# Kernel optimization log

Measured on AMD Instinct MI355X. Metric: run time of the kernel, lower is better.

The kernel has to match this reference:

```python
import jax, jax.numpy as jnp
import numpy as np

L = 4
VOCAB = 258  # 256 codes + 2 (pad/cls)
D = 512
B, T = 64, 1024


def setup_inputs() -> dict:
    key = jax.random.key(0)
    k1, k2, k3, k4 = jax.random.split(key, 4)
    level_ids = jax.random.randint(k1, (B, T), 0, L, dtype=jnp.int64)
    token_ids = jax.random.randint(k2, (B, T), 0, VOCAB, dtype=jnp.int64)
    # per-level embedding tables stacked: [L, VOCAB, D] (all vocab sizes equal)
    emb_tables = jax.random.normal(k3, (L, VOCAB, D), dtype=jnp.float32)
    level_embed = jax.random.normal(k4, (L, D), dtype=jnp.float32)
    return {"level_ids": level_ids, "token_ids": token_ids,
            "emb_tables": emb_tables, "level_embed": level_embed}


def reference(level_ids, token_ids, emb_tables, level_embed):
    # Fused form of the per-level masked gather/scatter: each (b,t) position
    # reads row token_ids[b,t] from table level_ids[b,t], then adds the
    # level embedding for that level. Dropout p=0.0 -> identity.
    out = emb_tables[level_ids, token_ids] + level_embed[level_ids]  # [B,T,D]
    return out
```

## Files before the change

kernel.cpp:

```cpp
#include <hip/hip_runtime.h>


#define MLE_D     512
#define MLE_D4    128
#define MLE_VOCAB 258

__global__ __launch_bounds__(256) void MultiLevelEmbedding_34437047780006_kernel(
    const int* __restrict__ level_ids,
    const int* __restrict__ token_ids,
    const float* __restrict__ emb_tables,
    const float* __restrict__ level_embed,
    float* __restrict__ out,
    long long total_f4)
{
    long long stride = (long long)gridDim.x * blockDim.x;
    for (long long i = (long long)blockIdx.x * blockDim.x + threadIdx.x;
         i < total_f4; i += stride) {
        int row = (int)(i >> 7);
        int d4  = (int)(i & 127);
        int lvl = level_ids[row];
        int tok = token_ids[row];
        const float4* tab = reinterpret_cast<const float4*>(
            emb_tables + ((long long)lvl * MLE_VOCAB + (long long)tok) * MLE_D);
        const float4* lev = reinterpret_cast<const float4*>(
            level_embed + (long long)lvl * MLE_D);
        float4 a = tab[d4];
        float4 b = lev[d4];
        float4 o;
        o.x = a.x + b.x;
        o.y = a.y + b.y;
        o.z = a.z + b.z;
        o.w = a.w + b.w;
        reinterpret_cast<float4*>(out)[i] = o;
    }
}

extern "C" void kernel_launch(void* const* d_in, const int* in_sizes, int n_in,
                              void* d_out, int out_size, void* d_ws, size_t ws_size,
                              hipStream_t stream) {
    const int*   level_ids   = (const int*)d_in[0];
    const int*   token_ids   = (const int*)d_in[1];
    const float* emb_tables  = (const float*)d_in[2];
    const float* level_embed = (const float*)d_in[3];
    float*       out         = (float*)d_out;

    int n_rows = in_sizes[0];
    long long total_f4 = (long long)n_rows * MLE_D4;

    const int block = 256;
    long long want_blocks = (total_f4 + block - 1) / block;
    int grid = (int)(want_blocks < 2048 ? want_blocks : 2048);

    MultiLevelEmbedding_34437047780006_kernel<<<grid, block, 0, stream>>>(
        level_ids, token_ids, emb_tables, level_embed, out, total_f4);
}
```

Baseline: 31.91 us.

## Map one wavefront per row with scalar index loads and nontemporal stores

Restructures the gather so each 64-lane wavefront handles a whole 512-float row, with the level and token ids read once and broadcast through readfirstlane instead of being reloaded per float4. The loop is unrolled to process two rows per iteration so more loads are in flight, and output writes use nontemporal stores to avoid polluting the cache. Total traffic is about 128MB of writes plus table reads that mostly hit in cache, so the kernel is write-bound and the expected gain is limited.

```diff
diff --git a/kernel.cpp b/kernel.cpp
--- a/kernel.cpp
+++ b/kernel.cpp
@@ -5,33 +5,67 @@
 #define MLE_D4    128
 #define MLE_VOCAB 258
 
+typedef float f32x4 __attribute__((ext_vector_type(4)));
+
 __global__ __launch_bounds__(256) void MultiLevelEmbedding_34437047780006_kernel(
     const int* __restrict__ level_ids,
     const int* __restrict__ token_ids,
     const float* __restrict__ emb_tables,
     const float* __restrict__ level_embed,
     float* __restrict__ out,
-    long long total_f4)
+    int nrows)
 {
-    long long stride = (long long)gridDim.x * blockDim.x;
-    for (long long i = (long long)blockIdx.x * blockDim.x + threadIdx.x;
-         i < total_f4; i += stride) {
-        int row = (int)(i >> 7);
-        int d4  = (int)(i & 127);
-        int lvl = level_ids[row];
-        int tok = token_ids[row];
-        const float4* tab = reinterpret_cast<const float4*>(
-            emb_tables + ((long long)lvl * MLE_VOCAB + (long long)tok) * MLE_D);
-        const float4* lev = reinterpret_cast<const float4*>(
-            level_embed + (long long)lvl * MLE_D);
-        float4 a = tab[d4];
-        float4 b = lev[d4];
-        float4 o;
-        o.x = a.x + b.x;
-        o.y = a.y + b.y;
-        o.z = a.z + b.z;
-        o.w = a.w + b.w;
-        reinterpret_cast<float4*>(out)[i] = o;
+    const int lane = (int)(threadIdx.x & 63);
+    const int wib  = __builtin_amdgcn_readfirstlane((int)(threadIdx.x >> 6));
+    const int nw   = (int)gridDim.x * 4;
+    int gw = (int)blockIdx.x * 4 + wib;
+
+    const f32x4* __restrict__ levv = reinterpret_cast<const f32x4*>(level_embed);
+
+    int row = gw;
+    for (; row + nw < nrows; row += 2 * nw) {
+        const int r0 = row;
+        const int r1 = row + nw;
+        const int lvl0 = __builtin_amdgcn_readfirstlane(level_ids[r0]);
+        const int tok0 = __builtin_amdgcn_readfirstlane(token_ids[r0]);
+        const int lvl1 = __builtin_amdgcn_readfirstlane(level_ids[r1]);
+        const int tok1 = __builtin_amdgcn_readfirstlane(token_ids[r1]);
+
+        const f32x4* __restrict__ t0 = reinterpret_cast<const f32x4*>(
+            emb_tables + (long long)(lvl0 * MLE_VOCAB + tok0) * MLE_D);
+        const f32x4* __restrict__ t1 = reinterpret_cast<const f32x4*>(
+            emb_tables + (long long)(lvl1 * MLE_VOCAB + tok1) * MLE_D);
+
+        f32x4 a0 = t0[lane];
+        f32x4 b0 = t0[lane + 64];
+        f32x4 a1 = t1[lane];
+        f32x4 b1 = t1[lane + 64];
+
+        f32x4 la0 = levv[lvl0 * MLE_D4 + lane];
+        f32x4 lb0 = levv[lvl0 * MLE_D4 + lane + 64];
+        f32x4 la1 = levv[lvl1 * MLE_D4 + lane];
+        f32x4 lb1 = levv[lvl1 * MLE_D4 + lane + 64];
+
+        f32x4* __restrict__ o0 = reinterpret_cast<f32x4*>(out + (long long)r0 * MLE_D);
+        f32x4* __restrict__ o1 = reinterpret_cast<f32x4*>(out + (long long)r1 * MLE_D);
+
+        __builtin_nontemporal_store(a0 + la0, o0 + lane);
+        __builtin_nontemporal_store(b0 + lb0, o0 + lane + 64);
+        __builtin_nontemporal_store(a1 + la1, o1 + lane);
+        __builtin_nontemporal_store(b1 + lb1, o1 + lane + 64);
+    }
+    for (; row < nrows; row += nw) {
+        const int lvl = __builtin_amdgcn_readfirstlane(level_ids[row]);
+        const int tok = __builtin_amdgcn_readfirstlane(token_ids[row]);
+        const f32x4* __restrict__ t = reinterpret_cast<const f32x4*>(
+            emb_tables + (long long)(lvl * MLE_VOCAB + tok) * MLE_D);
+        f32x4 a = t[lane];
+        f32x4 b = t[lane + 64];
+        f32x4 la = levv[lvl * MLE_D4 + lane];
+        f32x4 lb = levv[lvl * MLE_D4 + lane + 64];
+        f32x4* __restrict__ o = reinterpret_cast<f32x4*>(out + (long long)row * MLE_D);
+        __builtin_nontemporal_store(a + la, o + lane);
+        __builtin_nontemporal_store(b + lb, o + lane + 64);
     }
 }
 
@@ -44,13 +78,13 @@
     const float* level_embed = (const float*)d_in[3];
     float*       out         = (float*)d_out;
 
-    int n_rows = in_sizes[0];
-    long long total_f4 = (long long)n_rows * MLE_D4;
+    const int nrows = in_sizes[0];
 
     const int block = 256;
-    long long want_blocks = (total_f4 + block - 1) / block;
-    int grid = (int)(want_blocks < 2048 ? want_blocks : 2048);
+    int grid = 2048;
+    int max_blocks = (nrows + 3) / 4;
+    if (grid > max_blocks) grid = max_blocks;
 
     MultiLevelEmbedding_34437047780006_kernel<<<grid, block, 0, stream>>>(
-        level_ids, token_ids, emb_tables, level_embed, out, total_f4);
+        level_ids, token_ids, emb_tables, level_embed, out, nrows);
 }
```

Result: faster. 27.38 us, median of 2 (-14.2%).
